# Optimization experiments

Hardware: AMD Instinct MI355X
Metric: run time of the kernel (lower is better)

## Reference

```python
import jax, jax.numpy as jnp
import numpy as np

# ---- static config (matches init_kwargs) ----
IN_DIM = 1024
HIDDEN = 4096
U_OUT = 4
PROJ = HIDDEN // U_OUT          # 1024
BS = 64                          # block_size
NB = IN_DIM // BS                # 16 blocks (in == mid == out padded dims)
NRE = 3                          # n_reuploads
RANK = 64
EPS = 1e-5

# fixed stride permutation: arange.view(NB,BS).t().reshape(-1); mid_dim == in_padded so no pad/repeat
PERM = np.arange(NB * BS).reshape(NB, BS).T.reshape(-1)  # [1024]


def setup_inputs() -> dict:
    key = jax.random.key(0)
    ks = jax.random.split(key, 12)
    x = jax.random.normal(ks[0], (4, 2048, IN_DIM), dtype=jnp.float32)
    R = jax.random.normal(ks[1], (NB, BS, BS), dtype=jnp.float32) / jnp.sqrt(BS * 1.0)
    L = jax.random.normal(ks[2], (NB, BS, BS), dtype=jnp.float32) / jnp.sqrt(BS * 1.0)
    bias = jnp.zeros((PROJ,), jnp.float32)
    gamma = jnp.ones((PROJ,), jnp.float32)
    beta = jnp.zeros((PROJ,), jnp.float32)
    Wd = jax.random.normal(ks[3], (PROJ, RANK), dtype=jnp.float32) * 0.01   # down: dim->rank
    Wu = jax.random.normal(ks[4], (RANK, PROJ), dtype=jnp.float32) * 0.01   # up: rank->dim (torch init=0; nonzero for grad coverage)
    thetas = jnp.ones((NRE, PROJ), jnp.float32) + 0.1 * jax.random.normal(ks[5], (NRE, PROJ), dtype=jnp.float32)
    phis = 0.1 * jax.random.normal(ks[6], (NRE, PROJ), dtype=jnp.float32)
    Wp = jax.random.normal(ks[7], (U_OUT, 2 * NRE), dtype=jnp.float32) / jnp.sqrt(2.0 * NRE)
    bp = jnp.zeros((U_OUT,), jnp.float32)
    return {"x": x, "R": R, "L": L, "bias": bias, "gamma": gamma, "beta": beta,
            "Wd": Wd, "Wu": Wu, "thetas": thetas, "phis": phis, "Wp": Wp, "bp": bp}


def reference(x, R, L, bias, gamma, beta, Wd, Wu, thetas, phis, Wp, bp):
    B, S, _ = x.shape
    N = B * S
    # ---- MonarchProj: block-diag R, stride permute, block-diag L ----
    h = x.reshape(N, NB, BS)
    h = jnp.einsum('nbi,bij->nbj', h, R).reshape(N, NB * BS)
    h = h[:, PERM].reshape(N, NB, BS)
    h = jnp.einsum('nbi,bij->nbj', h, L).reshape(N, NB * BS)
    h = (h + bias).reshape(B, S, PROJ)
    # ---- LayerNorm ----
    mu = h.mean(-1, keepdims=True)
    var = ((h - mu) ** 2).mean(-1, keepdims=True)
    h = (h - mu) * jax.lax.rsqrt(var + EPS) * gamma + beta
    # ---- low-rank entangle: x + up(down(x)) ----
    h = h + (h @ Wd) @ Wu
    # ---- per-reupload rotation, interleaved sin/cos stacked on last dim ----
    rot = h[..., None] * thetas.T + phis.T                    # [B,S,PROJ,NRE]
    sc = jnp.stack([jnp.sin(rot), jnp.cos(rot)], axis=-1)     # [B,S,PROJ,NRE,2]
    sc = sc.reshape(B, S, PROJ, 2 * NRE)                      # [s0,c0,s1,c1,s2,c2]
    # ---- tiny final Linear then flatten ----
    out = sc @ Wp.T + bp                                      # [B,S,PROJ,U_OUT]
    return out.reshape(B, S, HIDDEN)
```

## Files before the change

### kernel.cpp

```cpp
#include <hip/hip_runtime.h>


typedef __attribute__((ext_vector_type(8))) short bf16x8;
typedef __attribute__((ext_vector_type(4))) float f32x4;

#define PITCH 1032
#define DPITCH 68
#define DHALF (16 * DPITCH)
#define SMEM_BYTES 75904

__device__ __forceinline__ unsigned short f2bf(float f) {
    unsigned u = __float_as_uint(f);
    u = (u + 0x7FFFu + ((u >> 16) & 1u)) >> 16;
    return (unsigned short)u;
}
__device__ __forceinline__ float bf2f(unsigned short h) {
    return __uint_as_float(((unsigned)h) << 16);
}
__device__ __forceinline__ void split_bf(float f, unsigned short &hi, unsigned short &lo) {
    hi = f2bf(f);
    lo = f2bf(f - bf2f(hi));
}
__device__ __forceinline__ f32x4 MFMA(bf16x8 a, bf16x8 b, f32x4 c) {
    return __builtin_amdgcn_mfma_f32_16x16x32_bf16(a, b, c, 0, 0, 0);
}

__global__ __launch_bounds__(256) void pack_weights(
    const float* __restrict__ R, const float* __restrict__ L,
    const float* __restrict__ Wd, const float* __restrict__ Wu,
    const float* __restrict__ gamma, const float* __restrict__ beta,
    unsigned short* __restrict__ wsp)
{
    const int blk = blockIdx.x;
    const int tid = threadIdx.x;
    if (blk == 64) {
        __shared__ float red[8][64];
        const int r = tid & 63, part = tid >> 6;
        float sb = 0.f, sc = 0.f;
        for (int c = part * 256; c < part * 256 + 256; ++c) {
            const float w = Wd[(size_t)c * 64 + r];
            sb += gamma[c] * w;
            sc += beta[c] * w;
        }
        red[part][r] = sb; red[part + 4][r] = sc;
        __syncthreads();
        if (part == 0) {
            float* bc = (float*)(wsp + (size_t)64 * 8192);
            bc[r]      = red[0][r] + red[1][r] + red[2][r] + red[3][r];
            bc[64 + r] = red[4][r] + red[5][r] + red[6][r] + red[7][r];
        }
        return;
    }
    unsigned short* dst = wsp + (size_t)blk * 8192;
    for (int it = 0; it < 4; ++it) {
        const int slot = tid + it * 256;
        const int fragidx = slot >> 6;
        const int l = slot & 63;
        const int kk = fragidx >> 3;
        const int nt = (fragidx >> 1) & 3;
        const int comp = fragidx & 1;
        const int g = l >> 4, r16 = l & 15;
        const int j = nt * 16 + r16;
        bf16x8 s;
        #pragma unroll
        for (int v = 0; v < 8; ++v) {
            const int k = kk * 32 + g * 8 + v;
            float w;
            if (blk < 16)      w = R[(size_t)blk * 4096 + k * 64 + j];
            else if (blk < 32) w = L[(size_t)(blk - 16) * 4096 + k * 64 + j];
            else if (blk < 48) {
                const int kglob = (blk - 32) * 64 + k;
                w = gamma[kglob] * Wd[(size_t)kglob * 64 + j];
            } else             w = Wu[(size_t)k * 1024 + (blk - 48) * 64 + j];
            unsigned short hi = f2bf(w);
            unsigned short bits = (comp == 0) ? hi : f2bf(w - bf2f(hi));
            s[v] = (short)bits;
        }
        *(bf16x8*)(dst + fragidx * 512 + l * 8) = s;
    }
}

__global__ __launch_bounds__(512, 4) void qrun_main(
    const float* __restrict__ x, const float* __restrict__ bias,
    const float* __restrict__ gamma, const float* __restrict__ beta,
    const float* __restrict__ thetas, const float* __restrict__ phis,
    const float* __restrict__ Wp, const float* __restrict__ bpv,
    const unsigned short* __restrict__ wpk, float* __restrict__ out)
{
    extern __shared__ char smem[];
    unsigned short* hiP = (unsigned short*)smem;
    unsigned short* loP = hiP + 16 * PITCH;
    float* dbuf = (float*)(loP + 16 * PITCH);
    float* lnpart = dbuf + 2 * DHALF;
    float* statsR = lnpart + 256;

    const int tid = threadIdx.x;
    const int wave = tid >> 6, lane = tid & 63;
    const int g = lane >> 4, r16 = lane & 15;
    const int grp = wave >> 2, ntw = wave & 3;
    const size_t n0 = (size_t)blockIdx.x * 16;
    const int rowA = r16 * PITCH;

    {
        #pragma unroll
        for (int it = 0; it < 4; ++it) {
            const int base = (it * 512 + tid) * 8;
            const int row = base >> 10, col = base & 1023;
            const float4 f0 = *(const float4*)(x + n0 * 1024 + base);
            const float4 f1 = *(const float4*)(x + n0 * 1024 + base + 4);
            bf16x8 hv, lv;
            unsigned short hh, ll;
            split_bf(f0.x, hh, ll); hv[0] = (short)hh; lv[0] = (short)ll;
            split_bf(f0.y, hh, ll); hv[1] = (short)hh; lv[1] = (short)ll;
            split_bf(f0.z, hh, ll); hv[2] = (short)hh; lv[2] = (short)ll;
            split_bf(f0.w, hh, ll); hv[3] = (short)hh; lv[3] = (short)ll;
            split_bf(f1.x, hh, ll); hv[4] = (short)hh; lv[4] = (short)ll;
            split_bf(f1.y, hh, ll); hv[5] = (short)hh; lv[5] = (short)ll;
            split_bf(f1.z, hh, ll); hv[6] = (short)hh; lv[6] = (short)ll;
            split_bf(f1.w, hh, ll); hv[7] = (short)hh; lv[7] = (short)ll;
            *(bf16x8*)(hiP + row * PITCH + col) = hv;
            *(bf16x8*)(loP + row * PITCH + col) = lv;
        }
    }
    __syncthreads();

    f32x4 acc1[8];
    #pragma unroll
    for (int bi = 0; bi < 8; ++bi) {
        const int b = grp * 8 + bi;
        const unsigned short* wb = wpk + (size_t)b * 8192;
        bf16x8 Bh0 = *(const bf16x8*)(wb + ((0*4+ntw)*2+0)*512 + lane*8);
        bf16x8 Bl0 = *(const bf16x8*)(wb + ((0*4+ntw)*2+1)*512 + lane*8);
        bf16x8 Bh1 = *(const bf16x8*)(wb + ((1*4+ntw)*2+0)*512 + lane*8);
        bf16x8 Bl1 = *(const bf16x8*)(wb + ((1*4+ntw)*2+1)*512 + lane*8);
        const int ca = b * 64 + g * 8;
        bf16x8 Ah0 = *(const bf16x8*)(hiP + rowA + ca);
        bf16x8 Al0 = *(const bf16x8*)(loP + rowA + ca);
        bf16x8 Ah1 = *(const bf16x8*)(hiP + rowA + ca + 32);
        bf16x8 Al1 = *(const bf16x8*)(loP + rowA + ca + 32);
        f32x4 a = {0.f, 0.f, 0.f, 0.f};
        a = MFMA(Ah0, Bh0, a); a = MFMA(Ah0, Bl0, a); a = MFMA(Al0, Bh0, a);
        a = MFMA(Ah1, Bh1, a); a = MFMA(Ah1, Bl1, a); a = MFMA(Al1, Bh1, a);
        acc1[bi] = a;
    }
    __syncthreads();

    {
        const int Cw = (ntw * 4 + (r16 >> 2)) * 64 + ((r16 >> 1) & 1) * 32
                     + (((grp + 2 * (r16 & 1)) ^ (r16 >> 2)) << 3);
        #pragma unroll
        for (int v = 0; v < 4; ++v) {
            const int rowv = (g * 4 + v) * PITCH;
            bf16x8 hv, lv;
            #pragma unroll
            for (int bi = 0; bi < 8; ++bi) {
                unsigned short hh, ll;
                split_bf(acc1[bi][v], hh, ll);
                hv[bi] = (short)hh; lv[bi] = (short)ll;
            }
            *(bf16x8*)(hiP + rowv + Cw) = hv;
            *(bf16x8*)(loP + rowv + Cw) = lv;
        }
    }
    __syncthreads();

    f32x4 acc2[8];
    #pragma unroll
    for (int ci = 0; ci < 8; ++ci) {
        const int c = grp * 8 + ci;
        const unsigned short* wb = wpk + (size_t)(16 + c) * 8192;
        bf16x8 Wh0 = *(const bf16x8*)(wb + ((0*4+ntw)*2+0)*512 + lane*8);
        bf16x8 Wl0 = *(const bf16x8*)(wb + ((0*4+ntw)*2+1)*512 + lane*8);
        bf16x8 Wh1 = *(const bf16x8*)(wb + ((1*4+ntw)*2+0)*512 + lane*8);
        bf16x8 Wl1 = *(const bf16x8*)(wb + ((1*4+ntw)*2+1)*512 + lane*8);
        const int gx = ((g ^ (c & 3)) << 3);
        const int c0 = rowA + c * 64 + gx;
        const int c1 = c0 + 32;
        bf16x8 Hh0 = *(const bf16x8*)(hiP + c0);
        bf16x8 Hl0 = *(const bf16x8*)(loP + c0);
        bf16x8 Hh1 = *(const bf16x8*)(hiP + c1);
        bf16x8 Hl1 = *(const bf16x8*)(loP + c1);
        f32x4 a = {0.f, 0.f, 0.f, 0.f};
        a = MFMA(Wh0, Hh0, a); a = MFMA(Wh0, Hl0, a); a = MFMA(Wl0, Hh0, a);
        a = MFMA(Wh1, Hh1, a); a = MFMA(Wh1, Hl1, a); a = MFMA(Wl1, Hh1, a);
        acc2[ci] = a;
    }
    __syncthreads();

    {
        float s = 0.f, s2 = 0.f;
        #pragma unroll
        for (int ci = 0; ci < 8; ++ci) {
            const int c = grp * 8 + ci;
            const int ncol = c * 64 + ntw * 16 + g * 4;
            const float4 bv = *(const float4*)(bias + ncol);
            float f0 = acc2[ci][0] + bv.x, f1 = acc2[ci][1] + bv.y;
            float f2 = acc2[ci][2] + bv.z, f3 = acc2[ci][3] + bv.w;
            s += f0 + f1 + f2 + f3;
            s2 += f0*f0 + f1*f1 + f2*f2 + f3*f3;
            ushort4 h4, l4;
            split_bf(f0, h4.x, l4.x); split_bf(f1, h4.y, l4.y);
            split_bf(f2, h4.z, l4.z); split_bf(f3, h4.w, l4.w);
            *(ushort4*)(hiP + rowA + ncol) = h4;
            *(ushort4*)(loP + rowA + ncol) = l4;
        }
        s  += __shfl_xor(s, 16);  s  += __shfl_xor(s, 32);
        s2 += __shfl_xor(s2, 16); s2 += __shfl_xor(s2, 32);
        if (g == 0) {
            lnpart[(wave * 16 + r16) * 2]     = s;
            lnpart[(wave * 16 + r16) * 2 + 1] = s2;
        }
    }
    __syncthreads();

    {
        if (tid < 16) {
            float s = 0.f, s2 = 0.f;
            #pragma unroll
            for (int w = 0; w < 8; ++w) {
                s  += lnpart[(w * 16 + tid) * 2];
                s2 += lnpart[(w * 16 + tid) * 2 + 1];
            }
            const float mu = s * (1.f / 1024.f);
            statsR[tid * 2]     = mu;
            statsR[tid * 2 + 1] = rsqrtf(s2 * (1.f / 1024.f) - mu * mu + 1e-5f);
        }
        f32x4 accd = {0.f, 0.f, 0.f, 0.f};
        #pragma unroll
        for (int ki = 0; ki < 16; ++ki) {
            const int kq = grp * 16 + ki;
            const int kb = kq >> 1, kin = kq & 1;
            const unsigned short* wb = wpk + (size_t)(32 + kb) * 8192;
            bf16x8 Wh = *(const bf16x8*)(wb + ((kin*4+ntw)*2+0)*512 + lane*8);
            bf16x8 Hh = *(const bf16x8*)(hiP + rowA + kq * 32 + g * 8);
            accd = MFMA(Wh, Hh, accd);
        }
        *(f32x4*)(dbuf + grp * DHALF + r16 * DPITCH + ntw * 16 + g * 4) = accd;
    }
    __syncthreads();

    const float muT = statsR[r16 * 2], rsT = statsR[r16 * 2 + 1];
    float muR[4], rsR[4];
    #pragma unroll
    for (int v = 0; v < 4; ++v) {
        muR[v] = statsR[(g * 4 + v) * 2];
        rsR[v] = statsR[(g * 4 + v) * 2 + 1];
    }
    const float* bc = (const float*)(wpk + (size_t)64 * 8192);
    bf16x8 dA[2];
    #pragma unroll
    for (int kk = 0; kk < 2; ++kk) {
        const int rb = kk * 32 + g * 8;
        const float4 B0 = *(const float4*)(bc + rb);
        const float4 B1 = *(const float4*)(bc + rb + 4);
        const float4 C0 = *(const float4*)(bc + 64 + rb);
        const float4 C1 = *(const float4*)(bc + 64 + rb + 4);
        const int di = r16 * DPITCH + rb;
        const f32x4 q0 = *(const f32x4*)(dbuf + di);
        const f32x4 q1 = *(const f32x4*)(dbuf + di + 4);
        const f32x4 p0 = *(const f32x4*)(dbuf + DHALF + di);
        const f32x4 p1 = *(const f32x4*)(dbuf + DHALF + di + 4);
        const float Ba[8] = {B0.x,B0.y,B0.z,B0.w,B1.x,B1.y,B1.z,B1.w};
        const float Ca[8] = {C0.x,C0.y,C0.z,C0.w,C1.x,C1.y,C1.z,C1.w};
        #pragma unroll
        for (int v = 0; v < 4; ++v) {
            const float d0 = rsT * (q0[v] + p0[v]) - muT * rsT * Ba[v]     + Ca[v];
            const float d1 = rsT * (q1[v] + p1[v]) - muT * rsT * Ba[v + 4] + Ca[v + 4];
            dA[kk][v]     = (short)f2bf(d0);
            dA[kk][v + 4] = (short)f2bf(d1);
        }
    }
    float wp[24];
    #pragma unroll
    for (int k2 = 0; k2 < 24; ++k2) wp[k2] = Wp[k2];
    const float bp0 = bpv[0], bp1 = bpv[1], bp2 = bpv[2], bp3 = bpv[3];
    float gpa[8], bpa[8];
    #pragma unroll
    for (int j = 0; j < 8; ++j) {
        const int p = (wave * 8 + j) * 16 + r16;
        gpa[j] = gamma[p]; bpa[j] = beta[p];
    }

    #pragma unroll 2
    for (int j = 0; j < 8; ++j) {
        const int ntg = wave * 8 + j;
        const int nb = ntg >> 2, ntin = ntg & 3;
        const unsigned short* wb = wpk + (size_t)(48 + nb) * 8192;
        bf16x8 Bh0 = *(const bf16x8*)(wb + ((0*4+ntin)*2+0)*512 + lane*8);
        bf16x8 Bh1 = *(const bf16x8*)(wb + ((1*4+ntin)*2+0)*512 + lane*8);
        f32x4 au = {0.f, 0.f, 0.f, 0.f};
        au = MFMA(dA[0], Bh0, au);
        au = MFMA(dA[1], Bh1, au);
        const int p = ntg * 16 + r16;
        const float th0 = thetas[p], th1 = thetas[1024 + p], th2 = thetas[2048 + p];
        const float ph0 = phis[p],   ph1 = phis[1024 + p],   ph2 = phis[2048 + p];
        #pragma unroll
        for (int v = 0; v < 4; ++v) {
            const int row = g * 4 + v;
            const float hraw = bf2f(hiP[row * PITCH + p]) + bf2f(loP[row * PITCH + p]);
            const float hn = (hraw - muR[v]) * rsR[v] * gpa[j] + bpa[j];
            const float e = au[v] + hn;
            float o0 = bp0, o1 = bp1, o2 = bp2, o3 = bp3;
            {
                const float rot = fmaf(e, th0, ph0);
                const float sn = __sinf(rot), cs = __cosf(rot);
                o0 = fmaf(sn, wp[0],  fmaf(cs, wp[1],  o0));
                o1 = fmaf(sn, wp[6],  fmaf(cs, wp[7],  o1));
                o2 = fmaf(sn, wp[12], fmaf(cs, wp[13], o2));
                o3 = fmaf(sn, wp[18], fmaf(cs, wp[19], o3));
            }
            {
                const float rot = fmaf(e, th1, ph1);
                const float sn = __sinf(rot), cs = __cosf(rot);
                o0 = fmaf(sn, wp[2],  fmaf(cs, wp[3],  o0));
                o1 = fmaf(sn, wp[8],  fmaf(cs, wp[9],  o1));
                o2 = fmaf(sn, wp[14], fmaf(cs, wp[15], o2));
                o3 = fmaf(sn, wp[20], fmaf(cs, wp[21], o3));
            }
            {
                const float rot = fmaf(e, th2, ph2);
                const float sn = __sinf(rot), cs = __cosf(rot);
                o0 = fmaf(sn, wp[4],  fmaf(cs, wp[5],  o0));
                o1 = fmaf(sn, wp[10], fmaf(cs, wp[11], o1));
                o2 = fmaf(sn, wp[16], fmaf(cs, wp[17], o2));
                o3 = fmaf(sn, wp[22], fmaf(cs, wp[23], o3));
            }
            *(float4*)(out + ((n0 + row) * 1024 + p) * 4) = make_float4(o0, o1, o2, o3);
        }
    }
}

extern "C" void kernel_launch(void* const* d_in, const int* in_sizes, int n_in,
                              void* d_out, int out_size, void* d_ws, size_t ws_size,
                              hipStream_t stream) {
    const float* x      = (const float*)d_in[0];
    const float* R      = (const float*)d_in[1];
    const float* L      = (const float*)d_in[2];
    const float* bias   = (const float*)d_in[3];
    const float* gamma  = (const float*)d_in[4];
    const float* beta   = (const float*)d_in[5];
    const float* Wd     = (const float*)d_in[6];
    const float* Wu     = (const float*)d_in[7];
    const float* thetas = (const float*)d_in[8];
    const float* phis   = (const float*)d_in[9];
    const float* Wp     = (const float*)d_in[10];
    const float* bp     = (const float*)d_in[11];
    float* out = (float*)d_out;
    unsigned short* wsp = (unsigned short*)d_ws;
    const int N = in_sizes[0] / 1024;

    (void)hipFuncSetAttribute((const void*)qrun_main,
                              hipFuncAttributeMaxDynamicSharedMemorySize, SMEM_BYTES);
    pack_weights<<<dim3(65), dim3(256), 0, stream>>>(R, L, Wd, Wu, gamma, beta, wsp);
    qrun_main<<<dim3(N / 16), dim3(512), SMEM_BYTES, stream>>>(
        x, bias, gamma, beta, thetas, phis, Wp, bp, wsp, out);
}
```

Baseline: 62.55 us.

## Process 32 tokens per block and use packed bf16 converts and hardware sin/cos

Each block now handles 32 tokens instead of 16, so every weight fragment loaded from global memory feeds two MFMA row tiles. This doubles LDS use and lowers occupancy to 2 blocks per CU. Scalar bf16 splitting is replaced with the packed v_cvt_pk_bf16_f32 instruction. Per-column gamma, beta, theta and phi are prepacked into one interleaved table, with theta and phi pre-scaled by 1/2π so the epilogue can call v_fract, v_sin and v_cos directly. The trade-off is fewer resident waves and slightly different range reduction in the trig path.

```diff
diff --git a/kernel.cpp b/kernel.cpp
--- a/kernel.cpp
+++ b/kernel.cpp
@@ -5,9 +5,9 @@
 typedef __attribute__((ext_vector_type(4))) float f32x4;
 
 #define PITCH 1032
+#define TOK 32
 #define DPITCH 68
-#define DHALF (16 * DPITCH)
-#define SMEM_BYTES 75904
+#define SMEM_BYTES 151808
 
 __device__ __forceinline__ unsigned short f2bf(float f) {
     unsigned u = __float_as_uint(f);
@@ -17,9 +17,16 @@
 __device__ __forceinline__ float bf2f(unsigned short h) {
     return __uint_as_float(((unsigned)h) << 16);
 }
-__device__ __forceinline__ void split_bf(float f, unsigned short &hi, unsigned short &lo) {
-    hi = f2bf(f);
-    lo = f2bf(f - bf2f(hi));
+__device__ __forceinline__ unsigned cvt_pk_bf16(float a, float b) {
+    unsigned r;
+    asm("v_cvt_pk_bf16_f32 %0, %1, %2" : "=v"(r) : "v"(a), "v"(b));
+    return r;
+}
+__device__ __forceinline__ void split2(float a, float b, unsigned &H, unsigned &L) {
+    H = cvt_pk_bf16(a, b);
+    const float ha = __uint_as_float(H << 16);
+    const float hb = __uint_as_float(H & 0xFFFF0000u);
+    L = cvt_pk_bf16(a - ha, b - hb);
 }
 __device__ __forceinline__ f32x4 MFMA(bf16x8 a, bf16x8 b, f32x4 c) {
     return __builtin_amdgcn_mfma_f32_16x16x32_bf16(a, b, c, 0, 0, 0);
@@ -29,11 +36,22 @@
     const float* __restrict__ R, const float* __restrict__ L,
     const float* __restrict__ Wd, const float* __restrict__ Wu,
     const float* __restrict__ gamma, const float* __restrict__ beta,
+    const float* __restrict__ thetas, const float* __restrict__ phis,
     unsigned short* __restrict__ wsp)
 {
     const int blk = blockIdx.x;
     const int tid = threadIdx.x;
     if (blk == 64) {
+        float* bc = (float*)(wsp + (size_t)64 * 8192);
+        const float INV2PI = 0.15915494309189535f;
+        for (int i = tid; i < 1024; i += 256) {
+            float* t = bc + 128 + i * 8;
+            t[0] = gamma[i];                 t[1] = beta[i];
+            t[2] = thetas[i] * INV2PI;       t[3] = thetas[1024 + i] * INV2PI;
+            t[4] = thetas[2048 + i] * INV2PI;
+            t[5] = phis[i] * INV2PI;         t[6] = phis[1024 + i] * INV2PI;
+            t[7] = phis[2048 + i] * INV2PI;
+        }
         __shared__ float red[8][64];
         const int r = tid & 63, part = tid >> 6;
         float sb = 0.f, sc = 0.f;
@@ -45,7 +63,6 @@
         red[part][r] = sb; red[part + 4][r] = sc;
         __syncthreads();
         if (part == 0) {
-            float* bc = (float*)(wsp + (size_t)64 * 8192);
             bc[r]      = red[0][r] + red[1][r] + red[2][r] + red[3][r];
             bc[64 + r] = red[4][r] + red[5][r] + red[6][r] + red[7][r];
         }
@@ -80,51 +97,44 @@
     }
 }
 
-__global__ __launch_bounds__(512, 4) void qrun_main(
+__global__ __launch_bounds__(512, 2) void qrun_main(
     const float* __restrict__ x, const float* __restrict__ bias,
-    const float* __restrict__ gamma, const float* __restrict__ beta,
-    const float* __restrict__ thetas, const float* __restrict__ phis,
     const float* __restrict__ Wp, const float* __restrict__ bpv,
     const unsigned short* __restrict__ wpk, float* __restrict__ out)
 {
     extern __shared__ char smem[];
     unsigned short* hiP = (unsigned short*)smem;
-    unsigned short* loP = hiP + 16 * PITCH;
-    float* dbuf = (float*)(loP + 16 * PITCH);
-    float* lnpart = dbuf + 2 * DHALF;
-    float* statsR = lnpart + 256;
+    unsigned short* loP = hiP + TOK * PITCH;
+    float* dbuf = (float*)(loP + TOK * PITCH);
+    float* lnpart = dbuf + 2 * TOK * DPITCH;
+    float* statsR = lnpart + 512;
 
     const int tid = threadIdx.x;
     const int wave = tid >> 6, lane = tid & 63;
     const int g = lane >> 4, r16 = lane & 15;
     const int grp = wave >> 2, ntw = wave & 3;
-    const size_t n0 = (size_t)blockIdx.x * 16;
-    const int rowA = r16 * PITCH;
+    const size_t n0 = (size_t)blockIdx.x * TOK;
 
     {
-        #pragma unroll
-        for (int it = 0; it < 4; ++it) {
+        const float* xb = x + n0 * 1024;
+        #pragma unroll
+        for (int it = 0; it < 8; ++it) {
             const int base = (it * 512 + tid) * 8;
             const int row = base >> 10, col = base & 1023;
-            const float4 f0 = *(const float4*)(x + n0 * 1024 + base);
-            const float4 f1 = *(const float4*)(x + n0 * 1024 + base + 4);
-            bf16x8 hv, lv;
-            unsigned short hh, ll;
-            split_bf(f0.x, hh, ll); hv[0] = (short)hh; lv[0] = (short)ll;
-            split_bf(f0.y, hh, ll); hv[1] = (short)hh; lv[1] = (short)ll;
-            split_bf(f0.z, hh, ll); hv[2] = (short)hh; lv[2] = (short)ll;
-            split_bf(f0.w, hh, ll); hv[3] = (short)hh; lv[3] = (short)ll;
-            split_bf(f1.x, hh, ll); hv[4] = (short)hh; lv[4] = (short)ll;
-            split_bf(f1.y, hh, ll); hv[5] = (short)hh; lv[5] = (short)ll;
-            split_bf(f1.z, hh, ll); hv[6] = (short)hh; lv[6] = (short)ll;
-            split_bf(f1.w, hh, ll); hv[7] = (short)hh; lv[7] = (short)ll;
-            *(bf16x8*)(hiP + row * PITCH + col) = hv;
-            *(bf16x8*)(loP + row * PITCH + col) = lv;
-        }
-    }
-    __syncthreads();
-
-    f32x4 acc1[8];
+            const float4 f0 = *(const float4*)(xb + base);
+            const float4 f1 = *(const float4*)(xb + base + 4);
+            unsigned H0, L0, H1, L1, H2, L2, H3, L3;
+            split2(f0.x, f0.y, H0, L0);
+            split2(f0.z, f0.w, H1, L1);
+            split2(f1.x, f1.y, H2, L2);
+            split2(f1.z, f1.w, H3, L3);
+            *(uint4*)(hiP + row * PITCH + col) = make_uint4(H0, H1, H2, H3);
+            *(uint4*)(loP + row * PITCH + col) = make_uint4(L0, L1, L2, L3);
+        }
+    }
+    __syncthreads();
+
+    f32x4 acc1[8][2];
     #pragma unroll
     for (int bi = 0; bi < 8; ++bi) {
         const int b = grp * 8 + bi;
@@ -134,14 +144,18 @@
         bf16x8 Bh1 = *(const bf16x8*)(wb + ((1*4+ntw)*2+0)*512 + lane*8);
         bf16x8 Bl1 = *(const bf16x8*)(wb + ((1*4+ntw)*2+1)*512 + lane*8);
         const int ca = b * 64 + g * 8;
-        bf16x8 Ah0 = *(const bf16x8*)(hiP + rowA + ca);
-        bf16x8 Al0 = *(const bf16x8*)(loP + rowA + ca);
-        bf16x8 Ah1 = *(const bf16x8*)(hiP + rowA + ca + 32);
-        bf16x8 Al1 = *(const bf16x8*)(loP + rowA + ca + 32);
-        f32x4 a = {0.f, 0.f, 0.f, 0.f};
-        a = MFMA(Ah0, Bh0, a); a = MFMA(Ah0, Bl0, a); a = MFMA(Al0, Bh0, a);
-        a = MFMA(Ah1, Bh1, a); a = MFMA(Ah1, Bl1, a); a = MFMA(Al1, Bh1, a);
-        acc1[bi] = a;
+        #pragma unroll
+        for (int tr = 0; tr < 2; ++tr) {
+            const int rowA = (tr * 16 + r16) * PITCH;
+            bf16x8 Ah0 = *(const bf16x8*)(hiP + rowA + ca);
+            bf16x8 Al0 = *(const bf16x8*)(loP + rowA + ca);
+            bf16x8 Ah1 = *(const bf16x8*)(hiP + rowA + ca + 32);
+            bf16x8 Al1 = *(const bf16x8*)(loP + rowA + ca + 32);
+            f32x4 a = {0.f, 0.f, 0.f, 0.f};
+            a = MFMA(Ah0, Bh0, a); a = MFMA(Ah0, Bl0, a); a = MFMA(Al0, Bh0, a);
+            a = MFMA(Ah1, Bh1, a); a = MFMA(Ah1, Bl1, a); a = MFMA(Al1, Bh1, a);
+            acc1[bi][tr] = a;
+        }
     }
     __syncthreads();
 
@@ -149,22 +163,23 @@
         const int Cw = (ntw * 4 + (r16 >> 2)) * 64 + ((r16 >> 1) & 1) * 32
                      + (((grp + 2 * (r16 & 1)) ^ (r16 >> 2)) << 3);
         #pragma unroll
-        for (int v = 0; v < 4; ++v) {
-            const int rowv = (g * 4 + v) * PITCH;
-            bf16x8 hv, lv;
-            #pragma unroll
-            for (int bi = 0; bi < 8; ++bi) {
-                unsigned short hh, ll;
-                split_bf(acc1[bi][v], hh, ll);
-                hv[bi] = (short)hh; lv[bi] = (short)ll;
-            }
-            *(bf16x8*)(hiP + rowv + Cw) = hv;
-            *(bf16x8*)(loP + rowv + Cw) = lv;
-        }
-    }
-    __syncthreads();
-
-    f32x4 acc2[8];
+        for (int tr = 0; tr < 2; ++tr) {
+            #pragma unroll
+            for (int v = 0; v < 4; ++v) {
+                const int rowv = (tr * 16 + g * 4 + v) * PITCH;
+                unsigned h0, l0, h1, l1, h2, l2, h3, l3;
+                split2(acc1[0][tr][v], acc1[1][tr][v], h0, l0);
+                split2(acc1[2][tr][v], acc1[3][tr][v], h1, l1);
+                split2(acc1[4][tr][v], acc1[5][tr][v], h2, l2);
+                split2(acc1[6][tr][v], acc1[7][tr][v], h3, l3);
+                *(uint4*)(hiP + rowv + Cw) = make_uint4(h0, h1, h2, h3);
+                *(uint4*)(loP + rowv + Cw) = make_uint4(l0, l1, l2, l3);
+            }
+        }
+    }
+    __syncthreads();
+
+    f32x4 acc2[8][2];
     #pragma unroll
     for (int ci = 0; ci < 8; ++ci) {
         const int c = grp * 8 + ci;
@@ -174,158 +189,181 @@
         bf16x8 Wh1 = *(const bf16x8*)(wb + ((1*4+ntw)*2+0)*512 + lane*8);
         bf16x8 Wl1 = *(const bf16x8*)(wb + ((1*4+ntw)*2+1)*512 + lane*8);
         const int gx = ((g ^ (c & 3)) << 3);
-        const int c0 = rowA + c * 64 + gx;
-        const int c1 = c0 + 32;
-        bf16x8 Hh0 = *(const bf16x8*)(hiP + c0);
-        bf16x8 Hl0 = *(const bf16x8*)(loP + c0);
-        bf16x8 Hh1 = *(const bf16x8*)(hiP + c1);
-        bf16x8 Hl1 = *(const bf16x8*)(loP + c1);
-        f32x4 a = {0.f, 0.f, 0.f, 0.f};
-        a = MFMA(Wh0, Hh0, a); a = MFMA(Wh0, Hl0, a); a = MFMA(Wl0, Hh0, a);
-        a = MFMA(Wh1, Hh1, a); a = MFMA(Wh1, Hl1, a); a = MFMA(Wl1, Hh1, a);
-        acc2[ci] = a;
+        #pragma unroll
+        for (int tr = 0; tr < 2; ++tr) {
+            const int c0 = (tr * 16 + r16) * PITCH + c * 64 + gx;
+            bf16x8 Hh0 = *(const bf16x8*)(hiP + c0);
+            bf16x8 Hl0 = *(const bf16x8*)(loP + c0);
+            bf16x8 Hh1 = *(const bf16x8*)(hiP + c0 + 32);
+            bf16x8 Hl1 = *(const bf16x8*)(loP + c0 + 32);
+            f32x4 a = {0.f, 0.f, 0.f, 0.f};
+            a = MFMA(Wh0, Hh0, a); a = MFMA(Wh0, Hl0, a); a = MFMA(Wl0, Hh0, a);
+            a = MFMA(Wh1, Hh1, a); a = MFMA(Wh1, Hl1, a); a = MFMA(Wl1, Hh1, a);
+            acc2[ci][tr] = a;
+        }
     }
     __syncthreads();
 
     {
+        #pragma unroll
+        for (int tr = 0; tr < 2; ++tr) {
+            const int rowA = (tr * 16 + r16) * PITCH;
+            float s = 0.f, s2 = 0.f;
+            #pragma unroll
+            for (int ci = 0; ci < 8; ++ci) {
+                const int c = grp * 8 + ci;
+                const int ncol = c * 64 + ntw * 16 + g * 4;
+                const float4 bv = *(const float4*)(bias + ncol);
+                const float f0 = acc2[ci][tr][0] + bv.x;
+                const float f1 = acc2[ci][tr][1] + bv.y;
+                const float f2 = acc2[ci][tr][2] + bv.z;
+                const float f3 = acc2[ci][tr][3] + bv.w;
+                s += f0 + f1 + f2 + f3;
+                s2 += f0 * f0 + f1 * f1 + f2 * f2 + f3 * f3;
+                unsigned hA, lA, hB, lB;
+                split2(f0, f1, hA, lA);
+                split2(f2, f3, hB, lB);
+                *(uint2*)(hiP + rowA + ncol) = make_uint2(hA, hB);
+                *(uint2*)(loP + rowA + ncol) = make_uint2(lA, lB);
+            }
+            s  += __shfl_xor(s, 16);  s  += __shfl_xor(s, 32);
+            s2 += __shfl_xor(s2, 16); s2 += __shfl_xor(s2, 32);
+            if (g == 0) {
+                const int e = ((wave * 2 + tr) * 16 + r16) * 2;
+                lnpart[e] = s; lnpart[e + 1] = s2;
+            }
+        }
+    }
+    __syncthreads();
+
+    if (tid < 32) {
         float s = 0.f, s2 = 0.f;
         #pragma unroll
-        for (int ci = 0; ci < 8; ++ci) {
-            const int c = grp * 8 + ci;
-            const int ncol = c * 64 + ntw * 16 + g * 4;
-            const float4 bv = *(const float4*)(bias + ncol);
-            float f0 = acc2[ci][0] + bv.x, f1 = acc2[ci][1] + bv.y;
-            float f2 = acc2[ci][2] + bv.z, f3 = acc2[ci][3] + bv.w;
-            s += f0 + f1 + f2 + f3;
-            s2 += f0*f0 + f1*f1 + f2*f2 + f3*f3;
-            ushort4 h4, l4;
-            split_bf(f0, h4.x, l4.x); split_bf(f1, h4.y, l4.y);
-            split_bf(f2, h4.z, l4.z); split_bf(f3, h4.w, l4.w);
-            *(ushort4*)(hiP + rowA + ncol) = h4;
-            *(ushort4*)(loP + rowA + ncol) = l4;
-        }
-        s  += __shfl_xor(s, 16);  s  += __shfl_xor(s, 32);
-        s2 += __shfl_xor(s2, 16); s2 += __shfl_xor(s2, 32);
-        if (g == 0) {
-            lnpart[(wave * 16 + r16) * 2]     = s;
-            lnpart[(wave * 16 + r16) * 2 + 1] = s2;
-        }
-    }
-    __syncthreads();
-
+        for (int w = 0; w < 8; ++w) {
+            const int e = ((w * 2 + (tid >> 4)) * 16 + (tid & 15)) * 2;
+            s += lnpart[e]; s2 += lnpart[e + 1];
+        }
+        const float mu = s * (1.f / 1024.f);
+        statsR[tid * 2]     = mu;
+        statsR[tid * 2 + 1] = rsqrtf(s2 * (1.f / 1024.f) - mu * mu + 1e-5f);
+    }
     {
-        if (tid < 16) {
-            float s = 0.f, s2 = 0.f;
-            #pragma unroll
-            for (int w = 0; w < 8; ++w) {
-                s  += lnpart[(w * 16 + tid) * 2];
-                s2 += lnpart[(w * 16 + tid) * 2 + 1];
-            }
-            const float mu = s * (1.f / 1024.f);
-            statsR[tid * 2]     = mu;
-            statsR[tid * 2 + 1] = rsqrtf(s2 * (1.f / 1024.f) - mu * mu + 1e-5f);
-        }
-        f32x4 accd = {0.f, 0.f, 0.f, 0.f};
+        f32x4 accd[2] = {{0.f,0.f,0.f,0.f}, {0.f,0.f,0.f,0.f}};
         #pragma unroll
         for (int ki = 0; ki < 16; ++ki) {
             const int kq = grp * 16 + ki;
             const int kb = kq >> 1, kin = kq & 1;
             const unsigned short* wb = wpk + (size_t)(32 + kb) * 8192;
             bf16x8 Wh = *(const bf16x8*)(wb + ((kin*4+ntw)*2+0)*512 + lane*8);
-            bf16x8 Hh = *(const bf16x8*)(hiP + rowA + kq * 32 + g * 8);
-            accd = MFMA(Wh, Hh, accd);
-        }
-        *(f32x4*)(dbuf + grp * DHALF + r16 * DPITCH + ntw * 16 + g * 4) = accd;
-    }
-    __syncthreads();
-
-    const float muT = statsR[r16 * 2], rsT = statsR[r16 * 2 + 1];
-    float muR[4], rsR[4];
-    #pragma unroll
-    for (int v = 0; v < 4; ++v) {
-        muR[v] = statsR[(g * 4 + v) * 2];
-        rsR[v] = statsR[(g * 4 + v) * 2 + 1];
-    }
-    const float* bc = (const float*)(wpk + (size_t)64 * 8192);
-    bf16x8 dA[2];
+            #pragma unroll
+            for (int tr = 0; tr < 2; ++tr) {
+                bf16x8 Hh = *(const bf16x8*)(hiP + (tr*16 + r16)*PITCH + kq*32 + g*8);
+                accd[tr] = MFMA(Wh, Hh, accd[tr]);
+            }
+        }
+        #pragma unroll
+        for (int tr = 0; tr < 2; ++tr)
+            *(f32x4*)(dbuf + (grp * 32 + tr * 16 + r16) * DPITCH + ntw * 16 + g * 4) = accd[tr];
+    }
+    __syncthreads();
+
+    const float* bcf = (const float*)(wpk + (size_t)64 * 8192);
+    float muT[2], rsT[2], muR[2][4], rsR[2][4];
+    #pragma unroll
+    for (int tr = 0; tr < 2; ++tr) {
+        muT[tr] = statsR[(tr * 16 + r16) * 2];
+        rsT[tr] = statsR[(tr * 16 + r16) * 2 + 1];
+        #pragma unroll
+        for (int v = 0; v < 4; ++v) {
+            muR[tr][v] = statsR[(tr * 16 + g * 4 + v) * 2];
+            rsR[tr][v] = statsR[(tr * 16 + g * 4 + v) * 2 + 1];
+        }
+    }
+    bf16x8 dA[2][2];
     #pragma unroll
     for (int kk = 0; kk < 2; ++kk) {
         const int rb = kk * 32 + g * 8;
-        const float4 B0 = *(const float4*)(bc + rb);
-        const float4 B1 = *(const float4*)(bc + rb + 4);
-        const float4 C0 = *(const float4*)(bc + 64 + rb);
-        const float4 C1 = *(const float4*)(bc + 64 + rb + 4);
-        const int di = r16 * DPITCH + rb;
-        const f32x4 q0 = *(const f32x4*)(dbuf + di);
-        const f32x4 q1 = *(const f32x4*)(dbuf + di + 4);
-        const f32x4 p0 = *(const f32x4*)(dbuf + DHALF + di);
-        const f32x4 p1 = *(const f32x4*)(dbuf + DHALF + di + 4);
+        const float4 B0 = *(const float4*)(bcf + rb);
+        const float4 B1 = *(const float4*)(bcf + rb + 4);
+        const float4 C0 = *(const float4*)(bcf + 64 + rb);
+        const float4 C1 = *(const float4*)(bcf + 64 + rb + 4);
         const float Ba[8] = {B0.x,B0.y,B0.z,B0.w,B1.x,B1.y,B1.z,B1.w};
         const float Ca[8] = {C0.x,C0.y,C0.z,C0.w,C1.x,C1.y,C1.z,C1.w};
         #pragma unroll
-        for (int v = 0; v < 4; ++v) {
-            const float d0 = rsT * (q0[v] + p0[v]) - muT * rsT * Ba[v]     + Ca[v];
-            const float d1 = rsT * (q1[v] + p1[v]) - muT * rsT * Ba[v + 4] + Ca[v + 4];
-            dA[kk][v]     = (short)f2bf(d0);
-            dA[kk][v + 4] = (short)f2bf(d1);
+        for (int tr = 0; tr < 2; ++tr) {
+            const int di = (tr * 16 + r16) * DPITCH + rb;
+            const f32x4 q0 = *(const f32x4*)(dbuf + di);
+            const f32x4 q1 = *(const f32x4*)(dbuf + di + 4);
+            const f32x4 p0 = *(const f32x4*)(dbuf + TOK * DPITCH + di);
+            const f32x4 p1 = *(const f32x4*)(dbuf + TOK * DPITCH + di + 4);
+            float dv[8];
+            #pragma unroll
+            for (int v = 0; v < 4; ++v) {
+                dv[v]     = rsT[tr] * (q0[v] + p0[v]) - muT[tr] * rsT[tr] * Ba[v]     + Ca[v];
+                dv[v + 4] = rsT[tr] * (q1[v] + p1[v]) - muT[tr] * rsT[tr] * Ba[v + 4] + Ca[v + 4];
+            }
+            const unsigned u0 = cvt_pk_bf16(dv[0], dv[1]);
+            const unsigned u1 = cvt_pk_bf16(dv[2], dv[3]);
+            const unsigned u2 = cvt_pk_bf16(dv[4], dv[5]);
+            const unsigned u3 = cvt_pk_bf16(dv[6], dv[7]);
+            uint4 uu = make_uint4(u0, u1, u2, u3);
+            dA[tr][kk] = *(bf16x8*)&uu;
         }
     }
     float wp[24];
     #pragma unroll
     for (int k2 = 0; k2 < 24; ++k2) wp[k2] = Wp[k2];
     const float bp0 = bpv[0], bp1 = bpv[1], bp2 = bpv[2], bp3 = bpv[3];
-    float gpa[8], bpa[8];
-    #pragma unroll
-    for (int j = 0; j < 8; ++j) {
-        const int p = (wave * 8 + j) * 16 + r16;
-        gpa[j] = gamma[p]; bpa[j] = beta[p];
-    }
-
-    #pragma unroll 2
+
+    #pragma unroll 1
     for (int j = 0; j < 8; ++j) {
         const int ntg = wave * 8 + j;
         const int nb = ntg >> 2, ntin = ntg & 3;
         const unsigned short* wb = wpk + (size_t)(48 + nb) * 8192;
         bf16x8 Bh0 = *(const bf16x8*)(wb + ((0*4+ntin)*2+0)*512 + lane*8);
         bf16x8 Bh1 = *(const bf16x8*)(wb + ((1*4+ntin)*2+0)*512 + lane*8);
-        f32x4 au = {0.f, 0.f, 0.f, 0.f};
-        au = MFMA(dA[0], Bh0, au);
-        au = MFMA(dA[1], Bh1, au);
         const int p = ntg * 16 + r16;
-        const float th0 = thetas[p], th1 = thetas[1024 + p], th2 = thetas[2048 + p];
-        const float ph0 = phis[p],   ph1 = phis[1024 + p],   ph2 = phis[2048 + p];
-        #pragma unroll
-        for (int v = 0; v < 4; ++v) {
-            const int row = g * 4 + v;
-            const float hraw = bf2f(hiP[row * PITCH + p]) + bf2f(loP[row * PITCH + p]);
-            const float hn = (hraw - muR[v]) * rsR[v] * gpa[j] + bpa[j];
-            const float e = au[v] + hn;
-            float o0 = bp0, o1 = bp1, o2 = bp2, o3 = bp3;
-            {
-                const float rot = fmaf(e, th0, ph0);
-                const float sn = __sinf(rot), cs = __cosf(rot);
+        const float4 t0 = *(const float4*)(bcf + 128 + p * 8);
+        const float4 t1 = *(const float4*)(bcf + 128 + p * 8 + 4);
+        const float gp = t0.x, bpp = t0.y;
+        const float th0 = t0.z, th1 = t0.w, th2 = t1.x;
+        const float ph0 = t1.y, ph1 = t1.z, ph2 = t1.w;
+        #pragma unroll
+        for (int tr = 0; tr < 2; ++tr) {
+            f32x4 au = {0.f, 0.f, 0.f, 0.f};
+            au = MFMA(dA[tr][0], Bh0, au);
+            au = MFMA(dA[tr][1], Bh1, au);
+            #pragma unroll
+            for (int v = 0; v < 4; ++v) {
+                const int row = tr * 16 + g * 4 + v;
+                const float hraw = bf2f(hiP[row * PITCH + p]) + bf2f(loP[row * PITCH + p]);
+                const float hn = (hraw - muR[tr][v]) * rsR[tr][v] * gp + bpp;
+                const float e = au[v] + hn;
+                float o0 = bp0, o1 = bp1, o2 = bp2, o3 = bp3;
+                float arg, sn, cs;
+                asm("v_fract_f32 %0, %1" : "=v"(arg) : "v"(fmaf(e, th0, ph0)));
+                asm("v_sin_f32 %0, %1" : "=v"(sn) : "v"(arg));
+                asm("v_cos_f32 %0, %1" : "=v"(cs) : "v"(arg));
                 o0 = fmaf(sn, wp[0],  fmaf(cs, wp[1],  o0));
                 o1 = fmaf(sn, wp[6],  fmaf(cs, wp[7],  o1));
                 o2 = fmaf(sn, wp[12], fmaf(cs, wp[13], o2));
                 o3 = fmaf(sn, wp[18], fmaf(cs, wp[19], o3));
-            }
-            {
-                const float rot = fmaf(e, th1, ph1);
-                const float sn = __sinf(rot), cs = __cosf(rot);
+                asm("v_fract_f32 %0, %1" : "=v"(arg) : "v"(fmaf(e, th1, ph1)));
+                asm("v_sin_f32 %0, %1" : "=v"(sn) : "v"(arg));
+                asm("v_cos_f32 %0, %1" : "=v"(cs) : "v"(arg));
                 o0 = fmaf(sn, wp[2],  fmaf(cs, wp[3],  o0));
                 o1 = fmaf(sn, wp[8],  fmaf(cs, wp[9],  o1));
                 o2 = fmaf(sn, wp[14], fmaf(cs, wp[15], o2));
                 o3 = fmaf(sn, wp[20], fmaf(cs, wp[21], o3));
-            }
-            {
-                const float rot = fmaf(e, th2, ph2);
-                const float sn = __sinf(rot), cs = __cosf(rot);
+                asm("v_fract_f32 %0, %1" : "=v"(arg) : "v"(fmaf(e, th2, ph2)));
+                asm("v_sin_f32 %0, %1" : "=v"(sn) : "v"(arg));
+                asm("v_cos_f32 %0, %1" : "=v"(cs) : "v"(arg));
                 o0 = fmaf(sn, wp[4],  fmaf(cs, wp[5],  o0));
                 o1 = fmaf(sn, wp[10], fmaf(cs, wp[11], o1));
                 o2 = fmaf(sn, wp[16], fmaf(cs, wp[17], o2));
                 o3 = fmaf(sn, wp[22], fmaf(cs, wp[23], o3));
-            }
-            *(float4*)(out + ((n0 + row) * 1024 + p) * 4) = make_float4(o0, o1, o2, o3);
+                *(float4*)(out + ((n0 + row) * 1024 + p) * 4) = make_float4(o0, o1, o2, o3);
+            }
         }
     }
 }
@@ -351,7 +389,8 @@
 
     (void)hipFuncSetAttribute((const void*)qrun_main,
                               hipFuncAttributeMaxDynamicSharedMemorySize, SMEM_BYTES);
-    pack_weights<<<dim3(65), dim3(256), 0, stream>>>(R, L, Wd, Wu, gamma, beta, wsp);
-    qrun_main<<<dim3(N / 16), dim3(512), SMEM_BYTES, stream>>>(
-        x, bias, gamma, beta, thetas, phis, Wp, bp, wsp, out);
-}
+    pack_weights<<<dim3(65), dim3(256), 0, stream>>>(R, L, Wd, Wu, gamma, beta,
+                                                     thetas, phis, wsp);
+    qrun_main<<<dim3(N / TOK), dim3(512), SMEM_BYTES, stream>>>(
+        x, bias, Wp, bp, wsp, out);
+}
```

New measurement: 63.99 us. 1.02x slower.
